# Kernel tuning notes

Hardware: AMD Instinct MI355X
Metric: run time of the kernel (lower is better)

## Reference

```python
import jax, jax.numpy as jnp
import numpy as np


def setup_inputs() -> dict:
    key = jax.random.key(0)
    k1, k2, k3 = jax.random.split(key, 3)
    N, C, Nf, W, H = 8, 256, 16, 28, 28
    l = jax.random.normal(k1, (N, C, Nf, W, H), dtype=jnp.float32)
    g = jax.random.normal(k2, (N, C, 1, 1, 1), dtype=jnp.float32)
    # 1x1x1 Conv3d(in=C, out=1, bias=False) weight collapses to a length-C vector
    w = jax.random.normal(k3, (C,), dtype=jnp.float32) * (1.0 / np.sqrt(C))
    return {"l": l, "g": g, "w": w}


def reference(l, g, w):
    # l: [N,C,Nf,W,H], g broadcastable to l, w: [C]
    N, C, Nf, W, H = l.shape
    # compatibility score: channel dot-product (1x1x1 conv, out_channels=1)
    c = jnp.einsum('ncfwh,c->nfwh', l + g, w)                      # [N,Nf,W,H]
    # softmax over the spatial dims (W*H) per frame, normalize_attn=True
    a = jax.nn.softmax(c.reshape(N, Nf, W * H), axis=-1)           # [N,Nf,WH]
    a = a.reshape(N, Nf, W, H)
    # attention-weighted spatial sum pooling -> [N,C,Nf]
    g_out = jnp.einsum('nfwh,ncfwh->ncf', a, l)
    # module returns raw compatibility map (pre-softmax) squeezed, and pooled g
    return (c, g_out)
```

## Files before the change

kernel.cpp:

```cpp
#include <hip/hip_runtime.h>
#include <math.h>

constexpr int N_ = 8, C_ = 256, F_ = 16, WH_ = 784;
constexpr int NF = N_ * F_;
constexpr int CH_STRIDE = F_ * WH_;
constexpr int SPLITS = 16;
constexpr int CPS = C_ / SPLITS;
constexpr int COUT_SZ = NF * WH_;
constexpr int P4 = WH_ / 4;

__device__ inline float wave_reduce_sum(float v) {
#pragma unroll
  for (int o = 32; o > 0; o >>= 1) v += __shfl_down(v, o, 64);
  return v;
}
__device__ inline float wave_reduce_max(float v) {
#pragma unroll
  for (int o = 32; o > 0; o >>= 1) v = fmaxf(v, __shfl_down(v, o, 64));
  return v;
}

__global__ __launch_bounds__(256) void k1_partial(
    const float* __restrict__ l, const float* __restrict__ w,
    float* __restrict__ part) {
  const int b = blockIdx.x;
  const int nf = b >> 4;
  const int s = b & 15;
  const int n = nf >> 4, f = nf & 15;
  const int t = threadIdx.x;
  if (t >= P4) return;

  const float* base = l + ((size_t)(n * C_ + s * CPS) * F_ + f) * WH_ + 4 * t;
  const float* wp = w + s * CPS;
  float4 acc = make_float4(0.f, 0.f, 0.f, 0.f);
#pragma unroll
  for (int j = 0; j < CPS; ++j) {
    const float wj = wp[j];
    const float4 v = *reinterpret_cast<const float4*>(base + (size_t)j * CH_STRIDE);
    acc.x = fmaf(v.x, wj, acc.x);
    acc.y = fmaf(v.y, wj, acc.y);
    acc.z = fmaf(v.z, wj, acc.z);
    acc.w = fmaf(v.w, wj, acc.w);
  }
  *reinterpret_cast<float4*>(part + (size_t)b * WH_ + 4 * t) = acc;
}

__global__ __launch_bounds__(256) void k2_softmax(
    const float* __restrict__ part, const float* __restrict__ g,
    const float* __restrict__ w, float* __restrict__ out,
    float* __restrict__ a) {
  __shared__ float red[4];
  __shared__ float bc;
  const int nf = blockIdx.x;
  const int n = nf >> 4;
  const int t = threadIdx.x;
  const int lane = t & 63, wv = t >> 6;

  float gv = g[n * C_ + t] * w[t];
  gv = wave_reduce_sum(gv);
  if (lane == 0) red[wv] = gv;
  __syncthreads();
  if (t == 0) bc = red[0] + red[1] + red[2] + red[3];
  __syncthreads();
  const float gb = bc;

  float4 cv = make_float4(-3.4e38f, -3.4e38f, -3.4e38f, -3.4e38f);
  if (t < P4) {
    const float* pp = part + (size_t)nf * SPLITS * WH_ + 4 * t;
    float4 s0 = make_float4(0.f, 0.f, 0.f, 0.f);
#pragma unroll
    for (int s = 0; s < SPLITS; ++s) {
      const float4 v = *reinterpret_cast<const float4*>(pp + (size_t)s * WH_);
      s0.x += v.x; s0.y += v.y; s0.z += v.z; s0.w += v.w;
    }
    cv = make_float4(s0.x + gb, s0.y + gb, s0.z + gb, s0.w + gb);
    *reinterpret_cast<float4*>(out + (size_t)nf * WH_ + 4 * t) = cv;
  }

  float m = fmaxf(fmaxf(cv.x, cv.y), fmaxf(cv.z, cv.w));
  m = wave_reduce_max(m);
  __syncthreads();
  if (lane == 0) red[wv] = m;
  __syncthreads();
  if (t == 0) bc = fmaxf(fmaxf(red[0], red[1]), fmaxf(red[2], red[3]));
  __syncthreads();
  const float cmax = bc;

  float4 e = make_float4(0.f, 0.f, 0.f, 0.f);
  if (t < P4) {
    e.x = expf(cv.x - cmax);
    e.y = expf(cv.y - cmax);
    e.z = expf(cv.z - cmax);
    e.w = expf(cv.w - cmax);
  }
  float ssum = (e.x + e.y) + (e.z + e.w);
  ssum = wave_reduce_sum(ssum);
  __syncthreads();
  if (lane == 0) red[wv] = ssum;
  __syncthreads();
  if (t == 0) bc = 1.f / (red[0] + red[1] + red[2] + red[3]);
  __syncthreads();
  const float inv = bc;

  if (t < P4) {
    e.x *= inv; e.y *= inv; e.z *= inv; e.w *= inv;
    *reinterpret_cast<float4*>(a + (size_t)nf * WH_ + 4 * t) = e;
  }
}

__global__ __launch_bounds__(256) void k3_pool(
    const float* __restrict__ l, const float* __restrict__ a,
    float* __restrict__ out) {
  const int b = blockIdx.x;
  const int n = b >> 8;
  const int f = (b >> 4) & 15;
  const int cg = b & 15;
  const int t = threadIdx.x, lane = t & 63, wv = t >> 6;
  const int p0 = lane << 2;

  const float* ar = a + ((size_t)n * F_ + f) * WH_;
  const float4 a0 = *reinterpret_cast<const float4*>(ar + p0);
  const float4 a1 = *reinterpret_cast<const float4*>(ar + p0 + 256);
  const float4 a2 = *reinterpret_cast<const float4*>(ar + p0 + 512);
  float4 a3 = make_float4(0.f, 0.f, 0.f, 0.f);
  if (lane < 4) a3 = *reinterpret_cast<const float4*>(ar + 768 + p0);

  const int c0 = cg * 16 + wv * 4;
#pragma unroll
  for (int k = 0; k < 4; ++k) {
    const int c = c0 + k;
    const float* lr = l + ((size_t)(n * C_ + c) * F_ + f) * WH_;
    const float4 x0 = *reinterpret_cast<const float4*>(lr + p0);
    const float4 x1 = *reinterpret_cast<const float4*>(lr + p0 + 256);
    const float4 x2 = *reinterpret_cast<const float4*>(lr + p0 + 512);
    float acc = 0.f;
    acc = fmaf(x0.x, a0.x, acc); acc = fmaf(x0.y, a0.y, acc);
    acc = fmaf(x0.z, a0.z, acc); acc = fmaf(x0.w, a0.w, acc);
    acc = fmaf(x1.x, a1.x, acc); acc = fmaf(x1.y, a1.y, acc);
    acc = fmaf(x1.z, a1.z, acc); acc = fmaf(x1.w, a1.w, acc);
    acc = fmaf(x2.x, a2.x, acc); acc = fmaf(x2.y, a2.y, acc);
    acc = fmaf(x2.z, a2.z, acc); acc = fmaf(x2.w, a2.w, acc);
    if (lane < 4) {
      const float4 x3 = *reinterpret_cast<const float4*>(lr + 768 + p0);
      acc = fmaf(x3.x, a3.x, acc); acc = fmaf(x3.y, a3.y, acc);
      acc = fmaf(x3.z, a3.z, acc); acc = fmaf(x3.w, a3.w, acc);
    }
    acc = wave_reduce_sum(acc);
    if (lane == 0) out[COUT_SZ + (size_t)(n * C_ + c) * F_ + f] = acc;
  }
}

extern "C" void kernel_launch(void* const* d_in, const int* in_sizes, int n_in,
                              void* d_out, int out_size, void* d_ws, size_t ws_size,
                              hipStream_t stream) {
  const float* l = (const float*)d_in[0];
  const float* g = (const float*)d_in[1];
  const float* w = (const float*)d_in[2];
  float* out = (float*)d_out;
  float* part = (float*)d_ws;
  float* a = part + (size_t)SPLITS * NF * WH_;

  k1_partial<<<dim3(NF * SPLITS), dim3(256), 0, stream>>>(l, w, part);
  k2_softmax<<<dim3(NF), dim3(256), 0, stream>>>(part, g, w, out, a);
  k3_pool<<<dim3(N_ * C_ * F_ / 16), dim3(256), 0, stream>>>(l, a, out);
}
```

Measured before the change: 168.3 us.

## Fuse three kernels into one persistent kernel with grid-wide barriers

Replaces the three separate launches (partial channel dot, softmax, pooling) with one 1024-block kernel that uses atomic-counter grid barriers between phases, plus a tiny init kernel to reset the counters. Splits are halved to 8 and each pooling block handles 32 channels instead of 16, so the block count matches the persistent grid. This removes inter-kernel launch gaps and lets all three phases share one launch. In exchange, only 128 blocks do work in the softmax phase while the rest spin, and correctness depends on all 1024 blocks being co-resident; the spin loop has a timeout that would break out silently if they are not.

Result: slower. 436.1 us (+159.2%).

```diff
diff --git a/kernel.cpp b/kernel.cpp
--- a/kernel.cpp
+++ b/kernel.cpp
@@ -4,10 +4,11 @@
 constexpr int N_ = 8, C_ = 256, F_ = 16, WH_ = 784;
 constexpr int NF = N_ * F_;
 constexpr int CH_STRIDE = F_ * WH_;
-constexpr int SPLITS = 16;
+constexpr int SPLITS = 8;
 constexpr int CPS = C_ / SPLITS;
 constexpr int COUT_SZ = NF * WH_;
 constexpr int P4 = WH_ / 4;
+constexpr unsigned GRID = 1024;
 
 __device__ inline float wave_reduce_sum(float v) {
 #pragma unroll
@@ -20,133 +21,151 @@
   return v;
 }
 
-__global__ __launch_bounds__(256) void k1_partial(
-    const float* __restrict__ l, const float* __restrict__ w,
-    float* __restrict__ part) {
-  const int b = blockIdx.x;
-  const int nf = b >> 4;
-  const int s = b & 15;
-  const int n = nf >> 4, f = nf & 15;
-  const int t = threadIdx.x;
-  if (t >= P4) return;
-
-  const float* base = l + ((size_t)(n * C_ + s * CPS) * F_ + f) * WH_ + 4 * t;
-  const float* wp = w + s * CPS;
-  float4 acc = make_float4(0.f, 0.f, 0.f, 0.f);
-#pragma unroll
-  for (int j = 0; j < CPS; ++j) {
-    const float wj = wp[j];
-    const float4 v = *reinterpret_cast<const float4*>(base + (size_t)j * CH_STRIDE);
-    acc.x = fmaf(v.x, wj, acc.x);
-    acc.y = fmaf(v.y, wj, acc.y);
-    acc.z = fmaf(v.z, wj, acc.z);
-    acc.w = fmaf(v.w, wj, acc.w);
+__device__ inline void grid_barrier(unsigned* bar, unsigned target) {
+  __syncthreads();
+  if (threadIdx.x == 0) {
+    __threadfence();
+    __hip_atomic_fetch_add(bar, 1u, __ATOMIC_ACQ_REL, __HIP_MEMORY_SCOPE_AGENT);
+    unsigned spins = 0;
+    while (__hip_atomic_load(bar, __ATOMIC_ACQUIRE, __HIP_MEMORY_SCOPE_AGENT) < target) {
+      __builtin_amdgcn_s_sleep(2);
+      if (++spins > (1u << 26)) break;
+    }
+    __threadfence();
   }
-  *reinterpret_cast<float4*>(part + (size_t)b * WH_ + 4 * t) = acc;
+  __syncthreads();
 }
 
-__global__ __launch_bounds__(256) void k2_softmax(
-    const float* __restrict__ part, const float* __restrict__ g,
+__global__ __launch_bounds__(64) void k_init(unsigned* bar) {
+  if (threadIdx.x < 2) bar[threadIdx.x] = 0u;
+}
+
+__global__ __launch_bounds__(256, 4) void mfla_fused(
+    const float* __restrict__ l, const float* __restrict__ g,
     const float* __restrict__ w, float* __restrict__ out,
-    float* __restrict__ a) {
+    float* __restrict__ part, float* __restrict__ a, unsigned* bar) {
   __shared__ float red[4];
   __shared__ float bc;
-  const int nf = blockIdx.x;
-  const int n = nf >> 4;
+  const int b = blockIdx.x;
   const int t = threadIdx.x;
   const int lane = t & 63, wv = t >> 6;
 
-  float gv = g[n * C_ + t] * w[t];
-  gv = wave_reduce_sum(gv);
-  if (lane == 0) red[wv] = gv;
-  __syncthreads();
-  if (t == 0) bc = red[0] + red[1] + red[2] + red[3];
-  __syncthreads();
-  const float gb = bc;
-
-  float4 cv = make_float4(-3.4e38f, -3.4e38f, -3.4e38f, -3.4e38f);
-  if (t < P4) {
-    const float* pp = part + (size_t)nf * SPLITS * WH_ + 4 * t;
-    float4 s0 = make_float4(0.f, 0.f, 0.f, 0.f);
-#pragma unroll
-    for (int s = 0; s < SPLITS; ++s) {
-      const float4 v = *reinterpret_cast<const float4*>(pp + (size_t)s * WH_);
-      s0.x += v.x; s0.y += v.y; s0.z += v.z; s0.w += v.w;
+  {
+    const int nf = b >> 3, s = b & 7;
+    const int n = nf >> 4, f = nf & 15;
+    if (t < P4) {
+      const float* base = l + ((size_t)(n * C_ + s * CPS) * F_ + f) * WH_ + 4 * t;
+      const float* wp = w + s * CPS;
+      float4 acc = make_float4(0.f, 0.f, 0.f, 0.f);
+#pragma unroll 8
+      for (int j = 0; j < CPS; ++j) {
+        const float wj = wp[j];
+        const float4 v = *reinterpret_cast<const float4*>(base + (size_t)j * CH_STRIDE);
+        acc.x = fmaf(v.x, wj, acc.x);
+        acc.y = fmaf(v.y, wj, acc.y);
+        acc.z = fmaf(v.z, wj, acc.z);
+        acc.w = fmaf(v.w, wj, acc.w);
+      }
+      *reinterpret_cast<float4*>(part + (size_t)b * WH_ + 4 * t) = acc;
     }
-    cv = make_float4(s0.x + gb, s0.y + gb, s0.z + gb, s0.w + gb);
-    *reinterpret_cast<float4*>(out + (size_t)nf * WH_ + 4 * t) = cv;
   }
 
-  float m = fmaxf(fmaxf(cv.x, cv.y), fmaxf(cv.z, cv.w));
-  m = wave_reduce_max(m);
-  __syncthreads();
-  if (lane == 0) red[wv] = m;
-  __syncthreads();
-  if (t == 0) bc = fmaxf(fmaxf(red[0], red[1]), fmaxf(red[2], red[3]));
-  __syncthreads();
-  const float cmax = bc;
+  grid_barrier(bar + 0, GRID);
 
-  float4 e = make_float4(0.f, 0.f, 0.f, 0.f);
-  if (t < P4) {
-    e.x = expf(cv.x - cmax);
-    e.y = expf(cv.y - cmax);
-    e.z = expf(cv.z - cmax);
-    e.w = expf(cv.w - cmax);
+  if (b < NF) {
+    const int nf = b;
+    const int n = nf >> 4;
+
+    float gv = g[n * C_ + t] * w[t];
+    gv = wave_reduce_sum(gv);
+    if (lane == 0) red[wv] = gv;
+    __syncthreads();
+    if (t == 0) bc = red[0] + red[1] + red[2] + red[3];
+    __syncthreads();
+    const float gb = bc;
+
+    float4 cv = make_float4(-3.4e38f, -3.4e38f, -3.4e38f, -3.4e38f);
+    if (t < P4) {
+      const float* pp = part + (size_t)nf * SPLITS * WH_ + 4 * t;
+      float4 s0 = make_float4(0.f, 0.f, 0.f, 0.f);
+#pragma unroll
+      for (int s = 0; s < SPLITS; ++s) {
+        const float4 v = *reinterpret_cast<const float4*>(pp + (size_t)s * WH_);
+        s0.x += v.x; s0.y += v.y; s0.z += v.z; s0.w += v.w;
+      }
+      cv = make_float4(s0.x + gb, s0.y + gb, s0.z + gb, s0.w + gb);
+      *reinterpret_cast<float4*>(out + (size_t)nf * WH_ + 4 * t) = cv;
+    }
+
+    float m = fmaxf(fmaxf(cv.x, cv.y), fmaxf(cv.z, cv.w));
+    m = wave_reduce_max(m);
+    __syncthreads();
+    if (lane == 0) red[wv] = m;
+    __syncthreads();
+    if (t == 0) bc = fmaxf(fmaxf(red[0], red[1]), fmaxf(red[2], red[3]));
+    __syncthreads();
+    const float cmax = bc;
+
+    float4 e = make_float4(0.f, 0.f, 0.f, 0.f);
+    if (t < P4) {
+      e.x = expf(cv.x - cmax);
+      e.y = expf(cv.y - cmax);
+      e.z = expf(cv.z - cmax);
+      e.w = expf(cv.w - cmax);
+    }
+    float ssum = (e.x + e.y) + (e.z + e.w);
+    ssum = wave_reduce_sum(ssum);
+    __syncthreads();
+    if (lane == 0) red[wv] = ssum;
+    __syncthreads();
+    if (t == 0) bc = 1.f / (red[0] + red[1] + red[2] + red[3]);
+    __syncthreads();
+    const float inv = bc;
+
+    if (t < P4) {
+      e.x *= inv; e.y *= inv; e.z *= inv; e.w *= inv;
+      *reinterpret_cast<float4*>(a + (size_t)nf * WH_ + 4 * t) = e;
+    }
   }
-  float ssum = (e.x + e.y) + (e.z + e.w);
-  ssum = wave_reduce_sum(ssum);
-  __syncthreads();
-  if (lane == 0) red[wv] = ssum;
-  __syncthreads();
-  if (t == 0) bc = 1.f / (red[0] + red[1] + red[2] + red[3]);
-  __syncthreads();
-  const float inv = bc;
 
-  if (t < P4) {
-    e.x *= inv; e.y *= inv; e.z *= inv; e.w *= inv;
-    *reinterpret_cast<float4*>(a + (size_t)nf * WH_ + 4 * t) = e;
-  }
-}
+  grid_barrier(bar + 1, GRID);
 
-__global__ __launch_bounds__(256) void k3_pool(
-    const float* __restrict__ l, const float* __restrict__ a,
-    float* __restrict__ out) {
-  const int b = blockIdx.x;
-  const int n = b >> 8;
-  const int f = (b >> 4) & 15;
-  const int cg = b & 15;
-  const int t = threadIdx.x, lane = t & 63, wv = t >> 6;
-  const int p0 = lane << 2;
+  {
+    const int n = b >> 7;
+    const int f = (b >> 3) & 15;
+    const int cg = b & 7;
+    const int p0 = lane << 2;
 
-  const float* ar = a + ((size_t)n * F_ + f) * WH_;
-  const float4 a0 = *reinterpret_cast<const float4*>(ar + p0);
-  const float4 a1 = *reinterpret_cast<const float4*>(ar + p0 + 256);
-  const float4 a2 = *reinterpret_cast<const float4*>(ar + p0 + 512);
-  float4 a3 = make_float4(0.f, 0.f, 0.f, 0.f);
-  if (lane < 4) a3 = *reinterpret_cast<const float4*>(ar + 768 + p0);
+    const float* ar = a + ((size_t)n * F_ + f) * WH_;
+    const float4 a0 = *reinterpret_cast<const float4*>(ar + p0);
+    const float4 a1 = *reinterpret_cast<const float4*>(ar + p0 + 256);
+    const float4 a2 = *reinterpret_cast<const float4*>(ar + p0 + 512);
+    float4 a3 = make_float4(0.f, 0.f, 0.f, 0.f);
+    if (lane < 4) a3 = *reinterpret_cast<const float4*>(ar + 768 + p0);
 
-  const int c0 = cg * 16 + wv * 4;
-#pragma unroll
-  for (int k = 0; k < 4; ++k) {
-    const int c = c0 + k;
-    const float* lr = l + ((size_t)(n * C_ + c) * F_ + f) * WH_;
-    const float4 x0 = *reinterpret_cast<const float4*>(lr + p0);
-    const float4 x1 = *reinterpret_cast<const float4*>(lr + p0 + 256);
-    const float4 x2 = *reinterpret_cast<const float4*>(lr + p0 + 512);
-    float acc = 0.f;
-    acc = fmaf(x0.x, a0.x, acc); acc = fmaf(x0.y, a0.y, acc);
-    acc = fmaf(x0.z, a0.z, acc); acc = fmaf(x0.w, a0.w, acc);
-    acc = fmaf(x1.x, a1.x, acc); acc = fmaf(x1.y, a1.y, acc);
-    acc = fmaf(x1.z, a1.z, acc); acc = fmaf(x1.w, a1.w, acc);
-    acc = fmaf(x2.x, a2.x, acc); acc = fmaf(x2.y, a2.y, acc);
-    acc = fmaf(x2.z, a2.z, acc); acc = fmaf(x2.w, a2.w, acc);
-    if (lane < 4) {
-      const float4 x3 = *reinterpret_cast<const float4*>(lr + 768 + p0);
-      acc = fmaf(x3.x, a3.x, acc); acc = fmaf(x3.y, a3.y, acc);
-      acc = fmaf(x3.z, a3.z, acc); acc = fmaf(x3.w, a3.w, acc);
+    const int c0 = cg * 32 + wv * 8;
+#pragma unroll 2
+    for (int k = 0; k < 8; ++k) {
+      const int c = c0 + k;
+      const float* lr = l + ((size_t)(n * C_ + c) * F_ + f) * WH_;
+      const float4 x0 = *reinterpret_cast<const float4*>(lr + p0);
+      const float4 x1 = *reinterpret_cast<const float4*>(lr + p0 + 256);
+      const float4 x2 = *reinterpret_cast<const float4*>(lr + p0 + 512);
+      float acc = 0.f;
+      acc = fmaf(x0.x, a0.x, acc); acc = fmaf(x0.y, a0.y, acc);
+      acc = fmaf(x0.z, a0.z, acc); acc = fmaf(x0.w, a0.w, acc);
+      acc = fmaf(x1.x, a1.x, acc); acc = fmaf(x1.y, a1.y, acc);
+      acc = fmaf(x1.z, a1.z, acc); acc = fmaf(x1.w, a1.w, acc);
+      acc = fmaf(x2.x, a2.x, acc); acc = fmaf(x2.y, a2.y, acc);
+      acc = fmaf(x2.z, a2.z, acc); acc = fmaf(x2.w, a2.w, acc);
+      if (lane < 4) {
+        const float4 x3 = *reinterpret_cast<const float4*>(lr + 768 + p0);
+        acc = fmaf(x3.x, a3.x, acc); acc = fmaf(x3.y, a3.y, acc);
+        acc = fmaf(x3.z, a3.z, acc); acc = fmaf(x3.w, a3.w, acc);
+      }
+      acc = wave_reduce_sum(acc);
+      if (lane == 0) out[COUT_SZ + (size_t)(n * C_ + c) * F_ + f] = acc;
     }
-    acc = wave_reduce_sum(acc);
-    if (lane == 0) out[COUT_SZ + (size_t)(n * C_ + c) * F_ + f] = acc;
   }
 }
 
@@ -159,8 +178,8 @@
   float* out = (float*)d_out;
   float* part = (float*)d_ws;
   float* a = part + (size_t)SPLITS * NF * WH_;
+  unsigned* bar = (unsigned*)(a + (size_t)NF * WH_);
 
-  k1_partial<<<dim3(NF * SPLITS), dim3(256), 0, stream>>>(l, w, part);
-  k2_softmax<<<dim3(NF), dim3(256), 0, stream>>>(part, g, w, out, a);
-  k3_pool<<<dim3(N_ * C_ * F_ / 16), dim3(256), 0, stream>>>(l, a, out);
+  k_init<<<dim3(1), dim3(64), 0, stream>>>(bar);
+  mfla_fused<<<dim3(GRID), dim3(256), 0, stream>>>(l, g, w, out, part, a, bar);
 }
```
